# Optimization experiments

Measured on AMD Instinct MI355X. Metric: run time of the kernel, lower is better.

Reference implementation:

```python
import jax, jax.numpy as jnp
import numpy as np

D_MODEL = 768
N_CH = 2
D_STATE = 16
RANK = 8
LORA_SCALE = 2.0  # alpha/rank = (rank*2.0)/rank
N_LOOPS = 4       # MAX_INFER_LOOPS
BATCH = 1
SEQ = 1024
EPS = 1e-6        # RMSNorm eps


def setup_inputs() -> dict:
    key = jax.random.key(0)
    ks = jax.random.split(key, 12)
    f32 = jnp.float32
    n = lambda k, shp, s: jax.random.normal(k, shp, dtype=f32) * s
    return {
        "x": jax.random.normal(ks[0], (BATCH, SEQ, D_MODEL), dtype=f32),
        "in_proj_base": n(ks[1], (N_CH * D_MODEL, D_MODEL), 0.02),
        "lora_A": n(ks[2], (RANK, D_MODEL), 0.05),
        "lora_B": n(ks[3], (N_CH * D_MODEL, RANK), 0.05),
        "A_theta": n(ks[4], (N_CH, D_MODEL, D_STATE), 0.1),
        "B_real": n(ks[5], (N_CH, D_MODEL, D_STATE), 0.1),
        "B_imag": n(ks[6], (N_CH, D_MODEL, D_STATE), 0.1),
        "C_real": n(ks[7], (N_CH, D_MODEL, D_STATE), 0.1),
        "C_imag": n(ks[8], (N_CH, D_MODEL, D_STATE), 0.1),
        "out_proj_w": n(ks[9], (D_MODEL, N_CH * D_MODEL), 0.02),
        "mixer_norm_w": jnp.ones((D_MODEL,), f32),
        "loop_norm_w": jnp.ones((D_MODEL,), f32),
        "step_emb": n(ks[10], (N_LOOPS, D_MODEL), 0.02),
    }


def _rmsnorm(v, w):
    return v * jax.lax.rsqrt(jnp.mean(v * v, axis=-1, keepdims=True) + EPS) * w


def reference(x, in_proj_base, lora_A, lora_B, A_theta, B_real, B_imag,
              C_real, C_imag, out_proj_w, mixer_norm_w, loop_norm_w, step_emb):
    Bsz, Lsz, d = x.shape
    # LoRA-merged in_proj weight: base + scale * (B @ A)  [loop-invariant]
    W_in = in_proj_base + LORA_SCALE * (lora_B @ lora_A)  # [2d, d]
    cos_t = jnp.cos(A_theta)[None, None]  # [1,1,ch,d,s]
    sin_t = jnp.sin(A_theta)[None, None]
    Br = B_real[None, None]; Bi = B_imag[None, None]
    Cr = C_real[None, None]; Ci = C_imag[None, None]
    real = jnp.zeros((Bsz, Lsz, N_CH, d, D_STATE), x.dtype)
    imag = jnp.zeros_like(real)
    for i in range(N_LOOPS):  # fixed outer reasoning loop
        h = x + step_emb[i]
        # Mamba3ReasoningBlock: in_proj -> complex rotation state update -> sum over d_state
        x_in = (h @ W_in.T).reshape(Bsz, Lsz, N_CH, d)[..., None]  # [B,L,ch,d,1]
        new_real = cos_t * real - sin_t * imag + Br * x_in
        new_imag = sin_t * real + cos_t * imag + Bi * x_in
        y = (Cr * new_real - Ci * new_imag).sum(-1).reshape(Bsz, Lsz, N_CH * d)
        out = _rmsnorm(y @ out_proj_w.T, mixer_norm_w)
        x = _rmsnorm(h + out, loop_norm_w)  # residual + loop_norm
        real, imag = new_real, new_imag
    return x
```

## Files before the change

kernel.cpp:

```cpp
#include <hip/hip_runtime.h>

#define D_MODEL   768
#define TWO_D     1536
#define SEQ       1024
#define N_LOOPS   4
#define RANK      8
#define D_STATE   16
#define EPS       1e-6f

typedef unsigned short u16;
typedef short s16x8 __attribute__((ext_vector_type(8)));
typedef unsigned short u16x4 __attribute__((ext_vector_type(4)));
typedef float f32x4 __attribute__((ext_vector_type(4)));

__device__ inline u16 f2bf(float f) {
    union { float f; unsigned u; } v; v.f = f;
    unsigned r = v.u + 0x7fffu + ((v.u >> 16) & 1u);
    return (u16)(r >> 16);
}
__device__ inline float bf2f(u16 b) {
    union { unsigned u; float f; } v; v.u = ((unsigned)b) << 16;
    return v.f;
}

__global__ __launch_bounds__(256) void prep_win(
    const float* __restrict__ base, const float* __restrict__ lA,
    const float* __restrict__ lB, u16* __restrict__ W)
{
    int idx = blockIdx.x * 256 + threadIdx.x;
    int r = idx / D_MODEL;
    int c = idx - r * D_MODEL;
    float acc = base[idx];
#pragma unroll
    for (int k = 0; k < RANK; ++k)
        acc += 2.0f * lB[r * RANK + k] * lA[k * D_MODEL + c];
    W[idx] = f2bf(acc);
}

__global__ __launch_bounds__(256) void prep_wout(
    const float* __restrict__ src, u16* __restrict__ dst)
{
    int i4 = blockIdx.x * 256 + threadIdx.x;
    const float4 v = *reinterpret_cast<const float4*>(src + (size_t)i4 * 4);
    u16x4 o; o.x = f2bf(v.x); o.y = f2bf(v.y); o.z = f2bf(v.z); o.w = f2bf(v.w);
    *reinterpret_cast<u16x4*>(dst + (size_t)i4 * 4) = o;
}

__global__ __launch_bounds__(256) void prep_g(
    const float* __restrict__ th, const float* __restrict__ Br,
    const float* __restrict__ Bi, const float* __restrict__ Cr,
    const float* __restrict__ Ci, float* __restrict__ G)
{
    int cd = blockIdx.x * 256 + threadIdx.x;
    if (cd >= TWO_D) return;
    float g0 = 0.f, g1 = 0.f, g2 = 0.f, g3 = 0.f;
    for (int s = 0; s < D_STATE; ++s) {
        int idx = cd * D_STATE + s;
        float t  = th[idx];
        float br = Br[idx], bi = Bi[idx];
        float cr = Cr[idx], ci = Ci[idx];
#pragma unroll
        for (int k = 0; k < 4; ++k) {
            float ck = cosf(k * t), sk = sinf(k * t);
            float er = ck * br - sk * bi;
            float ei = sk * br + ck * bi;
            float g  = cr * er - ci * ei;
            if (k == 0) g0 += g; else if (k == 1) g1 += g;
            else if (k == 2) g2 += g; else g3 += g;
        }
    }
    G[0 * TWO_D + cd] = g0;
    G[1 * TWO_D + cd] = g1;
    G[2 * TWO_D + cd] = g2;
    G[3 * TWO_D + cd] = g3;
}

__global__ __launch_bounds__(256) void init_h(
    const float* __restrict__ x, const float* __restrict__ emb,
    float* __restrict__ hf, u16* __restrict__ hb)
{
    int i4 = blockIdx.x * 256 + threadIdx.x;
    int base = i4 * 4;
    int d = base % D_MODEL;
    const float4 v = *reinterpret_cast<const float4*>(x + base);
    const float4 e = *reinterpret_cast<const float4*>(emb + d);
    float4 h = make_float4(v.x + e.x, v.y + e.y, v.z + e.z, v.w + e.w);
    *reinterpret_cast<float4*>(hf + base) = h;
    u16x4 o; o.x = f2bf(h.x); o.y = f2bf(h.y); o.z = f2bf(h.z); o.w = f2bf(h.w);
    *reinterpret_cast<u16x4*>(hb + base) = o;
}

template<int K, bool OUT_BF16>
__global__ __launch_bounds__(256) void gemm_nt(
    const u16* __restrict__ A, const u16* __restrict__ B,
    void* __restrict__ Cv, const int N)
{
    __shared__ u16 Al[64][72];
    __shared__ u16 Bl[64][72];
    const int t  = threadIdx.x;
    const int bm = blockIdx.y, bn = blockIdx.x;
    const int lane = t & 63, w = t >> 6;
    const int wr = w >> 1, wc = w & 1;
    const int lr = lane & 15, kg = lane >> 4;

    const int r0 = t >> 3;
    const int q0 = t & 7;
    const u16* Ag0 = A + (size_t)(bm * 64 + r0)      * K + q0 * 8;
    const u16* Ag1 = A + (size_t)(bm * 64 + r0 + 32) * K + q0 * 8;
    const u16* Bg0 = B + (size_t)(bn * 64 + r0)      * K + q0 * 8;
    const u16* Bg1 = B + (size_t)(bn * 64 + r0 + 32) * K + q0 * 8;

    uint4 ra0 = *reinterpret_cast<const uint4*>(Ag0);
    uint4 ra1 = *reinterpret_cast<const uint4*>(Ag1);
    uint4 rb0 = *reinterpret_cast<const uint4*>(Bg0);
    uint4 rb1 = *reinterpret_cast<const uint4*>(Bg1);

    f32x4 acc[2][2] = {};
    const int NKT = K / 64;
    for (int kt = 0; kt < NKT; ++kt) {
        *reinterpret_cast<uint4*>(&Al[r0][q0 * 8])      = ra0;
        *reinterpret_cast<uint4*>(&Al[r0 + 32][q0 * 8]) = ra1;
        *reinterpret_cast<uint4*>(&Bl[r0][q0 * 8])      = rb0;
        *reinterpret_cast<uint4*>(&Bl[r0 + 32][q0 * 8]) = rb1;
        __syncthreads();
        if (kt + 1 < NKT) {
            const int ko = (kt + 1) * 64;
            ra0 = *reinterpret_cast<const uint4*>(Ag0 + ko);
            ra1 = *reinterpret_cast<const uint4*>(Ag1 + ko);
            rb0 = *reinterpret_cast<const uint4*>(Bg0 + ko);
            rb1 = *reinterpret_cast<const uint4*>(Bg1 + ko);
        }
#pragma unroll
        for (int ks = 0; ks < 2; ++ks) {
            const int ko = ks * 32 + kg * 8;
            s16x8 a0 = *reinterpret_cast<const s16x8*>(&Al[wr * 32 + lr][ko]);
            s16x8 a1 = *reinterpret_cast<const s16x8*>(&Al[wr * 32 + 16 + lr][ko]);
            s16x8 b0 = *reinterpret_cast<const s16x8*>(&Bl[wc * 32 + lr][ko]);
            s16x8 b1 = *reinterpret_cast<const s16x8*>(&Bl[wc * 32 + 16 + lr][ko]);
            acc[0][0] = __builtin_amdgcn_mfma_f32_16x16x32_bf16(a0, b0, acc[0][0], 0, 0, 0);
            acc[0][1] = __builtin_amdgcn_mfma_f32_16x16x32_bf16(a0, b1, acc[0][1], 0, 0, 0);
            acc[1][0] = __builtin_amdgcn_mfma_f32_16x16x32_bf16(a1, b0, acc[1][0], 0, 0, 0);
            acc[1][1] = __builtin_amdgcn_mfma_f32_16x16x32_bf16(a1, b1, acc[1][1], 0, 0, 0);
        }
        __syncthreads();
    }
    const int crow0 = bm * 64 + wr * 32 + kg * 4;
    const int ccol0 = bn * 64 + wc * 32 + lr;
#pragma unroll
    for (int m = 0; m < 2; ++m)
#pragma unroll
        for (int n = 0; n < 2; ++n)
#pragma unroll
            for (int r = 0; r < 4; ++r) {
                const int row = crow0 + m * 16 + r;
                const int col = ccol0 + n * 16;
                const float v = acc[m][n][r];
                if (OUT_BF16) ((u16*)Cv)[(size_t)row * N + col] = f2bf(v);
                else          ((float*)Cv)[(size_t)row * N + col] = v;
            }
}

__global__ __launch_bounds__(256) void y_kernel(
    const u16* __restrict__ xin,
    const float* __restrict__ G,
    const int nacc, u16* __restrict__ y)
{
    int i4 = blockIdx.x * 256 + threadIdx.x;
    int base = i4 * 4;
    int cd = base % TWO_D;
    float s0 = 0.f, s1 = 0.f, s2 = 0.f, s3 = 0.f;
    for (int j = 0; j < nacc; ++j) {
        u16x4 v = *reinterpret_cast<const u16x4*>(&xin[(size_t)j * SEQ * TWO_D + base]);
        const float4 g = *reinterpret_cast<const float4*>(&G[(size_t)(nacc - 1 - j) * TWO_D + cd]);
        s0 += bf2f(v.x) * g.x; s1 += bf2f(v.y) * g.y;
        s2 += bf2f(v.z) * g.z; s3 += bf2f(v.w) * g.w;
    }
    u16x4 o; o.x = f2bf(s0); o.y = f2bf(s1); o.z = f2bf(s2); o.w = f2bf(s3);
    *reinterpret_cast<u16x4*>(&y[base]) = o;
}

__device__ inline float block_sum256(float v) {
    __shared__ float sm[4];
#pragma unroll
    for (int off = 32; off > 0; off >>= 1) v += __shfl_down(v, off, 64);
    __syncthreads();
    if ((threadIdx.x & 63) == 0) sm[threadIdx.x >> 6] = v;
    __syncthreads();
    return sm[0] + sm[1] + sm[2] + sm[3];
}

__global__ __launch_bounds__(256) void norm_kernel(
    const float* __restrict__ outpre,
    const float* __restrict__ hprev,
    const float* __restrict__ mw,
    const float* __restrict__ lw,
    const float* __restrict__ embn,
    float* __restrict__ dstf,
    u16* __restrict__ dstb)
{
    const int r = blockIdx.x;
    const int t = threadIdx.x;
    const size_t ro = (size_t)r * D_MODEL;
    float op[3], h[3];
    float ss = 0.f;
#pragma unroll
    for (int j = 0; j < 3; ++j) {
        int d = t + j * 256;
        op[j] = outpre[ro + d];
        h[j]  = hprev[ro + d];
        ss += op[j] * op[j];
    }
    ss = block_sum256(ss);
    const float rs1 = rsqrtf(ss * (1.0f / D_MODEL) + EPS);
    float tt[3];
    float ss2 = 0.f;
#pragma unroll
    for (int j = 0; j < 3; ++j) {
        int d = t + j * 256;
        tt[j] = h[j] + op[j] * rs1 * mw[d];
        ss2 += tt[j] * tt[j];
    }
    ss2 = block_sum256(ss2);
    const float rs2 = rsqrtf(ss2 * (1.0f / D_MODEL) + EPS);
#pragma unroll
    for (int j = 0; j < 3; ++j) {
        int d = t + j * 256;
        float xo = tt[j] * rs2 * lw[d];
        if (embn != nullptr) {
            float hn = xo + embn[d];
            dstf[ro + d] = hn;
            dstb[ro + d] = f2bf(hn);
        } else {
            dstf[ro + d] = xo;
        }
    }
}

extern "C" void kernel_launch(void* const* d_in, const int* in_sizes, int n_in,
                              void* d_out, int out_size, void* d_ws, size_t ws_size,
                              hipStream_t stream) {
    const float* x            = (const float*)d_in[0];
    const float* in_proj_base = (const float*)d_in[1];
    const float* lora_A       = (const float*)d_in[2];
    const float* lora_B       = (const float*)d_in[3];
    const float* A_theta      = (const float*)d_in[4];
    const float* B_real       = (const float*)d_in[5];
    const float* B_imag       = (const float*)d_in[6];
    const float* C_real       = (const float*)d_in[7];
    const float* C_imag       = (const float*)d_in[8];
    const float* out_proj_w   = (const float*)d_in[9];
    const float* mixer_w      = (const float*)d_in[10];
    const float* loop_w       = (const float*)d_in[11];
    const float* step_emb     = (const float*)d_in[12];
    float* out = (float*)d_out;

    char* p = (char*)d_ws;
    u16*   Wbf    = (u16*)p;                       p += (size_t)TWO_D * D_MODEL * 2;
    u16*   Woutbf = (u16*)p;                       p += (size_t)D_MODEL * TWO_D * 2;
    float* G      = (float*)p;                     p += (size_t)4 * TWO_D * 4;
    u16*   xin    = (u16*)p;                       p += (size_t)N_LOOPS * SEQ * TWO_D * 2;
    u16*   ybf    = (u16*)p;                       p += (size_t)SEQ * TWO_D * 2;
    float* hAf    = (float*)p;                     p += (size_t)SEQ * D_MODEL * 4;
    float* hBf    = (float*)p;                     p += (size_t)SEQ * D_MODEL * 4;
    u16*   hbf    = (u16*)p;                       p += (size_t)SEQ * D_MODEL * 2;
    float* outpre = (float*)p;                     p += (size_t)SEQ * D_MODEL * 4;

    prep_win<<<(TWO_D * D_MODEL) / 256, 256, 0, stream>>>(in_proj_base, lora_A, lora_B, Wbf);
    prep_wout<<<(D_MODEL * TWO_D / 4) / 256, 256, 0, stream>>>(out_proj_w, Woutbf);
    prep_g<<<(TWO_D + 255) / 256, 256, 0, stream>>>(A_theta, B_real, B_imag, C_real, C_imag, G);
    init_h<<<(SEQ * D_MODEL / 4) / 256, 256, 0, stream>>>(x, step_emb, hAf, hbf);

    float* hcur = hAf;
    float* hnxt = hBf;
    for (int i = 0; i < N_LOOPS; ++i) {
        const bool last = (i == N_LOOPS - 1);
        gemm_nt<D_MODEL, true><<<dim3(TWO_D / 64, SEQ / 64), 256, 0, stream>>>(
            hbf, Wbf, (void*)(xin + (size_t)i * SEQ * TWO_D), TWO_D);
        y_kernel<<<(SEQ * TWO_D / 4) / 256, 256, 0, stream>>>(xin, G, i + 1, ybf);
        gemm_nt<TWO_D, false><<<dim3(D_MODEL / 64, SEQ / 64), 256, 0, stream>>>(
            ybf, Woutbf, (void*)outpre, D_MODEL);
        norm_kernel<<<SEQ, 256, 0, stream>>>(
            outpre, hcur, mixer_w, loop_w,
            last ? nullptr : (step_emb + (size_t)(i + 1) * D_MODEL),
            last ? out : hnxt,
            last ? nullptr : hbf);
        float* tmp = hcur; hcur = hnxt; hnxt = tmp;
    }
}
```

Baseline: 244.5 us.

## Fuse prep kernels, fold y accumulation into GEMM1 epilogue, split-K GEMM2

Merges the four setup kernels into one launch, and folds the y recurrence into the epilogue of the in_proj GEMM so the separate y kernel disappears. Both GEMMs now use a 128-wide K tile with padded shared memory. The out_proj GEMM is split along K into two partial outputs that the norm kernel adds together, doubling its grid from 192 blocks to fill more CUs. In exchange there is an extra fp32 partial buffer, and the new epilogue does scalar strided reads of older xin slots and of G.

```diff
diff --git a/kernel.cpp b/kernel.cpp
--- a/kernel.cpp
+++ b/kernel.cpp
@@ -7,6 +7,8 @@
 #define RANK      8
 #define D_STATE   16
 #define EPS       1e-6f
+#define BK        128
+#define LDA       136
 
 typedef unsigned short u16;
 typedef short s16x8 __attribute__((ext_vector_type(8)));
@@ -23,120 +25,118 @@
     return v.f;
 }
 
-__global__ __launch_bounds__(256) void prep_win(
+__global__ __launch_bounds__(256) void prep_all(
     const float* __restrict__ base, const float* __restrict__ lA,
-    const float* __restrict__ lB, u16* __restrict__ W)
-{
-    int idx = blockIdx.x * 256 + threadIdx.x;
-    int r = idx / D_MODEL;
-    int c = idx - r * D_MODEL;
-    float acc = base[idx];
-#pragma unroll
-    for (int k = 0; k < RANK; ++k)
-        acc += 2.0f * lB[r * RANK + k] * lA[k * D_MODEL + c];
-    W[idx] = f2bf(acc);
-}
-
-__global__ __launch_bounds__(256) void prep_wout(
-    const float* __restrict__ src, u16* __restrict__ dst)
-{
-    int i4 = blockIdx.x * 256 + threadIdx.x;
-    const float4 v = *reinterpret_cast<const float4*>(src + (size_t)i4 * 4);
-    u16x4 o; o.x = f2bf(v.x); o.y = f2bf(v.y); o.z = f2bf(v.z); o.w = f2bf(v.w);
-    *reinterpret_cast<u16x4*>(dst + (size_t)i4 * 4) = o;
-}
-
-__global__ __launch_bounds__(256) void prep_g(
-    const float* __restrict__ th, const float* __restrict__ Br,
-    const float* __restrict__ Bi, const float* __restrict__ Cr,
-    const float* __restrict__ Ci, float* __restrict__ G)
-{
-    int cd = blockIdx.x * 256 + threadIdx.x;
-    if (cd >= TWO_D) return;
-    float g0 = 0.f, g1 = 0.f, g2 = 0.f, g3 = 0.f;
-    for (int s = 0; s < D_STATE; ++s) {
-        int idx = cd * D_STATE + s;
-        float t  = th[idx];
-        float br = Br[idx], bi = Bi[idx];
-        float cr = Cr[idx], ci = Ci[idx];
-#pragma unroll
-        for (int k = 0; k < 4; ++k) {
-            float ck = cosf(k * t), sk = sinf(k * t);
-            float er = ck * br - sk * bi;
-            float ei = sk * br + ck * bi;
-            float g  = cr * er - ci * ei;
-            if (k == 0) g0 += g; else if (k == 1) g1 += g;
-            else if (k == 2) g2 += g; else g3 += g;
-        }
-    }
-    G[0 * TWO_D + cd] = g0;
-    G[1 * TWO_D + cd] = g1;
-    G[2 * TWO_D + cd] = g2;
-    G[3 * TWO_D + cd] = g3;
-}
-
-__global__ __launch_bounds__(256) void init_h(
-    const float* __restrict__ x, const float* __restrict__ emb,
+    const float* __restrict__ lB,   const float* __restrict__ wout,
+    const float* __restrict__ x,    const float* __restrict__ emb0,
+    const float* __restrict__ th,   const float* __restrict__ Br,
+    const float* __restrict__ Bi,   const float* __restrict__ Cr,
+    const float* __restrict__ Ci,
+    u16* __restrict__ Wbf, u16* __restrict__ Woutbf, float* __restrict__ G,
     float* __restrict__ hf, u16* __restrict__ hb)
 {
-    int i4 = blockIdx.x * 256 + threadIdx.x;
-    int base = i4 * 4;
-    int d = base % D_MODEL;
-    const float4 v = *reinterpret_cast<const float4*>(x + base);
-    const float4 e = *reinterpret_cast<const float4*>(emb + d);
-    float4 h = make_float4(v.x + e.x, v.y + e.y, v.z + e.z, v.w + e.w);
-    *reinterpret_cast<float4*>(hf + base) = h;
-    u16x4 o; o.x = f2bf(h.x); o.y = f2bf(h.y); o.z = f2bf(h.z); o.w = f2bf(h.w);
-    *reinterpret_cast<u16x4*>(hb + base) = o;
-}
-
-template<int K, bool OUT_BF16>
-__global__ __launch_bounds__(256) void gemm_nt(
-    const u16* __restrict__ A, const u16* __restrict__ B,
-    void* __restrict__ Cv, const int N)
+    const int b = blockIdx.x, t = threadIdx.x;
+    if (b < 1152) {
+        int i0 = (b * 256 + t) * 4;
+        int r = i0 / D_MODEL, c = i0 % D_MODEL;
+        float4 a = *reinterpret_cast<const float4*>(&base[i0]);
+#pragma unroll
+        for (int k = 0; k < RANK; ++k) {
+            float bk = 2.0f * lB[r * RANK + k];
+            const float4 av = *reinterpret_cast<const float4*>(&lA[k * D_MODEL + c]);
+            a.x += bk * av.x; a.y += bk * av.y; a.z += bk * av.z; a.w += bk * av.w;
+        }
+        u16x4 o; o.x = f2bf(a.x); o.y = f2bf(a.y); o.z = f2bf(a.z); o.w = f2bf(a.w);
+        *reinterpret_cast<u16x4*>(&Wbf[i0]) = o;
+    } else if (b < 2304) {
+        int i0 = ((b - 1152) * 256 + t) * 4;
+        const float4 v = *reinterpret_cast<const float4*>(&wout[i0]);
+        u16x4 o; o.x = f2bf(v.x); o.y = f2bf(v.y); o.z = f2bf(v.z); o.w = f2bf(v.w);
+        *reinterpret_cast<u16x4*>(&Woutbf[i0]) = o;
+    } else if (b < 3072) {
+        int i0 = ((b - 2304) * 256 + t) * 4;
+        int d = i0 % D_MODEL;
+        const float4 v = *reinterpret_cast<const float4*>(&x[i0]);
+        const float4 e = *reinterpret_cast<const float4*>(&emb0[d]);
+        float4 h = make_float4(v.x + e.x, v.y + e.y, v.z + e.z, v.w + e.w);
+        *reinterpret_cast<float4*>(&hf[i0]) = h;
+        u16x4 o; o.x = f2bf(h.x); o.y = f2bf(h.y); o.z = f2bf(h.z); o.w = f2bf(h.w);
+        *reinterpret_cast<u16x4*>(&hb[i0]) = o;
+    } else {
+        int cd = (b - 3072) * 256 + t;
+        if (cd >= TWO_D) return;
+        float g0 = 0.f, g1 = 0.f, g2 = 0.f, g3 = 0.f;
+        for (int s = 0; s < D_STATE; ++s) {
+            int idx = cd * D_STATE + s;
+            float tt = th[idx];
+            float br = Br[idx], bi = Bi[idx];
+            float cr = Cr[idx], ci = Ci[idx];
+#pragma unroll
+            for (int k = 0; k < 4; ++k) {
+                float ck = cosf(k * tt), sk = sinf(k * tt);
+                float er = ck * br - sk * bi;
+                float ei = sk * br + ck * bi;
+                float g  = cr * er - ci * ei;
+                if (k == 0) g0 += g; else if (k == 1) g1 += g;
+                else if (k == 2) g2 += g; else g3 += g;
+            }
+        }
+        G[0 * TWO_D + cd] = g0; G[1 * TWO_D + cd] = g1;
+        G[2 * TWO_D + cd] = g2; G[3 * TWO_D + cd] = g3;
+    }
+}
+
+__global__ __launch_bounds__(256) void gemm1y_kernel(
+    const u16* __restrict__ A,
+    const u16* __restrict__ B,
+    u16* __restrict__ xin,
+    u16* __restrict__ ybf,
+    const float* __restrict__ G,
+    const int li)
 {
-    __shared__ u16 Al[64][72];
-    __shared__ u16 Bl[64][72];
-    const int t  = threadIdx.x;
-    const int bm = blockIdx.y, bn = blockIdx.x;
+    __shared__ __align__(16) u16 Al[64 * LDA];
+    __shared__ __align__(16) u16 Bl[64 * LDA];
+    const int K = D_MODEL;
+    const int t = threadIdx.x, bm = blockIdx.y, bn = blockIdx.x;
     const int lane = t & 63, w = t >> 6;
     const int wr = w >> 1, wc = w & 1;
     const int lr = lane & 15, kg = lane >> 4;
 
-    const int r0 = t >> 3;
-    const int q0 = t & 7;
-    const u16* Ag0 = A + (size_t)(bm * 64 + r0)      * K + q0 * 8;
-    const u16* Ag1 = A + (size_t)(bm * 64 + r0 + 32) * K + q0 * 8;
-    const u16* Bg0 = B + (size_t)(bn * 64 + r0)      * K + q0 * 8;
-    const u16* Bg1 = B + (size_t)(bn * 64 + r0 + 32) * K + q0 * 8;
-
-    uint4 ra0 = *reinterpret_cast<const uint4*>(Ag0);
-    uint4 ra1 = *reinterpret_cast<const uint4*>(Ag1);
-    uint4 rb0 = *reinterpret_cast<const uint4*>(Bg0);
-    uint4 rb1 = *reinterpret_cast<const uint4*>(Bg1);
-
+    const u16* Ab = A + (size_t)bm * 64 * K;
+    const u16* Bb = B + (size_t)bn * 64 * K;
+    uint4 pa[4], pb[4];
+#pragma unroll
+    for (int q = 0; q < 4; ++q) {
+        int gid = q * 256 + t, row = gid >> 4, g = gid & 15;
+        pa[q] = *reinterpret_cast<const uint4*>(Ab + (size_t)row * K + g * 8);
+        pb[q] = *reinterpret_cast<const uint4*>(Bb + (size_t)row * K + g * 8);
+    }
     f32x4 acc[2][2] = {};
-    const int NKT = K / 64;
+    const int NKT = K / BK;
     for (int kt = 0; kt < NKT; ++kt) {
-        *reinterpret_cast<uint4*>(&Al[r0][q0 * 8])      = ra0;
-        *reinterpret_cast<uint4*>(&Al[r0 + 32][q0 * 8]) = ra1;
-        *reinterpret_cast<uint4*>(&Bl[r0][q0 * 8])      = rb0;
-        *reinterpret_cast<uint4*>(&Bl[r0 + 32][q0 * 8]) = rb1;
+#pragma unroll
+        for (int q = 0; q < 4; ++q) {
+            int gid = q * 256 + t, row = gid >> 4, g = gid & 15;
+            *reinterpret_cast<uint4*>(&Al[row * LDA + g * 8]) = pa[q];
+            *reinterpret_cast<uint4*>(&Bl[row * LDA + g * 8]) = pb[q];
+        }
         __syncthreads();
         if (kt + 1 < NKT) {
-            const int ko = (kt + 1) * 64;
-            ra0 = *reinterpret_cast<const uint4*>(Ag0 + ko);
-            ra1 = *reinterpret_cast<const uint4*>(Ag1 + ko);
-            rb0 = *reinterpret_cast<const uint4*>(Bg0 + ko);
-            rb1 = *reinterpret_cast<const uint4*>(Bg1 + ko);
-        }
-#pragma unroll
-        for (int ks = 0; ks < 2; ++ks) {
-            const int ko = ks * 32 + kg * 8;
-            s16x8 a0 = *reinterpret_cast<const s16x8*>(&Al[wr * 32 + lr][ko]);
-            s16x8 a1 = *reinterpret_cast<const s16x8*>(&Al[wr * 32 + 16 + lr][ko]);
-            s16x8 b0 = *reinterpret_cast<const s16x8*>(&Bl[wc * 32 + lr][ko]);
-            s16x8 b1 = *reinterpret_cast<const s16x8*>(&Bl[wc * 32 + 16 + lr][ko]);
+            const int ko = (kt + 1) * BK;
+#pragma unroll
+            for (int q = 0; q < 4; ++q) {
+                int gid = q * 256 + t, row = gid >> 4, g = gid & 15;
+                pa[q] = *reinterpret_cast<const uint4*>(Ab + (size_t)row * K + ko + g * 8);
+                pb[q] = *reinterpret_cast<const uint4*>(Bb + (size_t)row * K + ko + g * 8);
+            }
+        }
+#pragma unroll
+        for (int ks = 0; ks < BK / 32; ++ks) {
+            const int co = ks * 32 + kg * 8;
+            s16x8 a0 = *reinterpret_cast<const s16x8*>(&Al[(wr * 32 +      lr) * LDA + co]);
+            s16x8 a1 = *reinterpret_cast<const s16x8*>(&Al[(wr * 32 + 16 + lr) * LDA + co]);
+            s16x8 b0 = *reinterpret_cast<const s16x8*>(&Bl[(wc * 32 +      lr) * LDA + co]);
+            s16x8 b1 = *reinterpret_cast<const s16x8*>(&Bl[(wc * 32 + 16 + lr) * LDA + co]);
             acc[0][0] = __builtin_amdgcn_mfma_f32_16x16x32_bf16(a0, b0, acc[0][0], 0, 0, 0);
             acc[0][1] = __builtin_amdgcn_mfma_f32_16x16x32_bf16(a0, b1, acc[0][1], 0, 0, 0);
             acc[1][0] = __builtin_amdgcn_mfma_f32_16x16x32_bf16(a1, b0, acc[1][0], 0, 0, 0);
@@ -146,37 +146,93 @@
     }
     const int crow0 = bm * 64 + wr * 32 + kg * 4;
     const int ccol0 = bn * 64 + wc * 32 + lr;
-#pragma unroll
-    for (int m = 0; m < 2; ++m)
-#pragma unroll
-        for (int n = 0; n < 2; ++n)
+    u16* xslot = xin + (size_t)li * SEQ * TWO_D;
+#pragma unroll
+    for (int n = 0; n < 2; ++n) {
+        const int col = ccol0 + n * 16;
+        const float g0 = G[col];
+#pragma unroll
+        for (int m = 0; m < 2; ++m)
 #pragma unroll
             for (int r = 0; r < 4; ++r) {
                 const int row = crow0 + m * 16 + r;
-                const int col = ccol0 + n * 16;
+                const size_t off = (size_t)row * TWO_D + col;
                 const float v = acc[m][n][r];
-                if (OUT_BF16) ((u16*)Cv)[(size_t)row * N + col] = f2bf(v);
-                else          ((float*)Cv)[(size_t)row * N + col] = v;
+                xslot[off] = f2bf(v);
+                float y = g0 * v;
+                for (int j = 0; j < li; ++j)
+                    y += G[(size_t)(li - j) * TWO_D + col] *
+                         bf2f(xin[(size_t)j * SEQ * TWO_D + off]);
+                ybf[off] = f2bf(y);
             }
-}
-
-__global__ __launch_bounds__(256) void y_kernel(
-    const u16* __restrict__ xin,
-    const float* __restrict__ G,
-    const int nacc, u16* __restrict__ y)
+    }
+}
+
+__global__ __launch_bounds__(256) void gemm2_kernel(
+    const u16* __restrict__ A,
+    const u16* __restrict__ B,
+    float* __restrict__ Cp)
 {
-    int i4 = blockIdx.x * 256 + threadIdx.x;
-    int base = i4 * 4;
-    int cd = base % TWO_D;
-    float s0 = 0.f, s1 = 0.f, s2 = 0.f, s3 = 0.f;
-    for (int j = 0; j < nacc; ++j) {
-        u16x4 v = *reinterpret_cast<const u16x4*>(&xin[(size_t)j * SEQ * TWO_D + base]);
-        const float4 g = *reinterpret_cast<const float4*>(&G[(size_t)(nacc - 1 - j) * TWO_D + cd]);
-        s0 += bf2f(v.x) * g.x; s1 += bf2f(v.y) * g.y;
-        s2 += bf2f(v.z) * g.z; s3 += bf2f(v.w) * g.w;
-    }
-    u16x4 o; o.x = f2bf(s0); o.y = f2bf(s1); o.z = f2bf(s2); o.w = f2bf(s3);
-    *reinterpret_cast<u16x4*>(&y[base]) = o;
+    __shared__ __align__(16) u16 Al[64 * LDA];
+    __shared__ __align__(16) u16 Bl[64 * LDA];
+    const int K = TWO_D;
+    const int t = threadIdx.x, bm = blockIdx.y, bn = blockIdx.x, kz = blockIdx.z;
+    const int lane = t & 63, w = t >> 6;
+    const int wr = w >> 1, wc = w & 1;
+    const int lr = lane & 15, kg = lane >> 4;
+
+    const u16* Ab = A + (size_t)bm * 64 * K + kz * (K / 2);
+    const u16* Bb = B + (size_t)bn * 64 * K + kz * (K / 2);
+    uint4 pa[4], pb[4];
+#pragma unroll
+    for (int q = 0; q < 4; ++q) {
+        int gid = q * 256 + t, row = gid >> 4, g = gid & 15;
+        pa[q] = *reinterpret_cast<const uint4*>(Ab + (size_t)row * K + g * 8);
+        pb[q] = *reinterpret_cast<const uint4*>(Bb + (size_t)row * K + g * 8);
+    }
+    f32x4 acc[2][2] = {};
+    const int NKT = (K / 2) / BK;
+    for (int kt = 0; kt < NKT; ++kt) {
+#pragma unroll
+        for (int q = 0; q < 4; ++q) {
+            int gid = q * 256 + t, row = gid >> 4, g = gid & 15;
+            *reinterpret_cast<uint4*>(&Al[row * LDA + g * 8]) = pa[q];
+            *reinterpret_cast<uint4*>(&Bl[row * LDA + g * 8]) = pb[q];
+        }
+        __syncthreads();
+        if (kt + 1 < NKT) {
+            const int ko = (kt + 1) * BK;
+#pragma unroll
+            for (int q = 0; q < 4; ++q) {
+                int gid = q * 256 + t, row = gid >> 4, g = gid & 15;
+                pa[q] = *reinterpret_cast<const uint4*>(Ab + (size_t)row * K + ko + g * 8);
+                pb[q] = *reinterpret_cast<const uint4*>(Bb + (size_t)row * K + ko + g * 8);
+            }
+        }
+#pragma unroll
+        for (int ks = 0; ks < BK / 32; ++ks) {
+            const int co = ks * 32 + kg * 8;
+            s16x8 a0 = *reinterpret_cast<const s16x8*>(&Al[(wr * 32 +      lr) * LDA + co]);
+            s16x8 a1 = *reinterpret_cast<const s16x8*>(&Al[(wr * 32 + 16 + lr) * LDA + co]);
+            s16x8 b0 = *reinterpret_cast<const s16x8*>(&Bl[(wc * 32 +      lr) * LDA + co]);
+            s16x8 b1 = *reinterpret_cast<const s16x8*>(&Bl[(wc * 32 + 16 + lr) * LDA + co]);
+            acc[0][0] = __builtin_amdgcn_mfma_f32_16x16x32_bf16(a0, b0, acc[0][0], 0, 0, 0);
+            acc[0][1] = __builtin_amdgcn_mfma_f32_16x16x32_bf16(a0, b1, acc[0][1], 0, 0, 0);
+            acc[1][0] = __builtin_amdgcn_mfma_f32_16x16x32_bf16(a1, b0, acc[1][0], 0, 0, 0);
+            acc[1][1] = __builtin_amdgcn_mfma_f32_16x16x32_bf16(a1, b1, acc[1][1], 0, 0, 0);
+        }
+        __syncthreads();
+    }
+    const int crow0 = bm * 64 + wr * 32 + kg * 4;
+    const int ccol0 = bn * 64 + wc * 32 + lr;
+    float* Cz = Cp + (size_t)kz * SEQ * D_MODEL;
+#pragma unroll
+    for (int m = 0; m < 2; ++m)
+#pragma unroll
+        for (int n = 0; n < 2; ++n)
+#pragma unroll
+            for (int r = 0; r < 4; ++r)
+                Cz[(size_t)(crow0 + m * 16 + r) * D_MODEL + ccol0 + n * 16] = acc[m][n][r];
 }
 
 __device__ inline float block_sum256(float v) {
@@ -190,13 +246,11 @@
 }
 
 __global__ __launch_bounds__(256) void norm_kernel(
-    const float* __restrict__ outpre,
+    const float* __restrict__ op0, const float* __restrict__ op1,
     const float* __restrict__ hprev,
-    const float* __restrict__ mw,
-    const float* __restrict__ lw,
+    const float* __restrict__ mw,  const float* __restrict__ lw,
     const float* __restrict__ embn,
-    float* __restrict__ dstf,
-    u16* __restrict__ dstb)
+    float* __restrict__ dstf, u16* __restrict__ dstb)
 {
     const int r = blockIdx.x;
     const int t = threadIdx.x;
@@ -206,7 +260,7 @@
 #pragma unroll
     for (int j = 0; j < 3; ++j) {
         int d = t + j * 256;
-        op[j] = outpre[ro + d];
+        op[j] = op0[ro + d] + op1[ro + d];
         h[j]  = hprev[ro + d];
         ss += op[j] * op[j];
     }
@@ -255,32 +309,31 @@
     float* out = (float*)d_out;
 
     char* p = (char*)d_ws;
-    u16*   Wbf    = (u16*)p;                       p += (size_t)TWO_D * D_MODEL * 2;
-    u16*   Woutbf = (u16*)p;                       p += (size_t)D_MODEL * TWO_D * 2;
-    float* G      = (float*)p;                     p += (size_t)4 * TWO_D * 4;
-    u16*   xin    = (u16*)p;                       p += (size_t)N_LOOPS * SEQ * TWO_D * 2;
-    u16*   ybf    = (u16*)p;                       p += (size_t)SEQ * TWO_D * 2;
-    float* hAf    = (float*)p;                     p += (size_t)SEQ * D_MODEL * 4;
-    float* hBf    = (float*)p;                     p += (size_t)SEQ * D_MODEL * 4;
-    u16*   hbf    = (u16*)p;                       p += (size_t)SEQ * D_MODEL * 2;
-    float* outpre = (float*)p;                     p += (size_t)SEQ * D_MODEL * 4;
-
-    prep_win<<<(TWO_D * D_MODEL) / 256, 256, 0, stream>>>(in_proj_base, lora_A, lora_B, Wbf);
-    prep_wout<<<(D_MODEL * TWO_D / 4) / 256, 256, 0, stream>>>(out_proj_w, Woutbf);
-    prep_g<<<(TWO_D + 255) / 256, 256, 0, stream>>>(A_theta, B_real, B_imag, C_real, C_imag, G);
-    init_h<<<(SEQ * D_MODEL / 4) / 256, 256, 0, stream>>>(x, step_emb, hAf, hbf);
+    u16*   Wbf    = (u16*)p;   p += (size_t)TWO_D * D_MODEL * 2;
+    u16*   Woutbf = (u16*)p;   p += (size_t)D_MODEL * TWO_D * 2;
+    float* G      = (float*)p; p += (size_t)4 * TWO_D * 4;
+    u16*   xin    = (u16*)p;   p += (size_t)N_LOOPS * SEQ * TWO_D * 2;
+    u16*   ybf    = (u16*)p;   p += (size_t)SEQ * TWO_D * 2;
+    float* hAf    = (float*)p; p += (size_t)SEQ * D_MODEL * 4;
+    float* hBf    = (float*)p; p += (size_t)SEQ * D_MODEL * 4;
+    u16*   hbf    = (u16*)p;   p += (size_t)SEQ * D_MODEL * 2;
+    float* outpre = (float*)p; p += (size_t)2 * SEQ * D_MODEL * 4;
+
+    prep_all<<<3078, 256, 0, stream>>>(
+        in_proj_base, lora_A, lora_B, out_proj_w, x, step_emb,
+        A_theta, B_real, B_imag, C_real, C_imag,
+        Wbf, Woutbf, G, hAf, hbf);
 
     float* hcur = hAf;
     float* hnxt = hBf;
     for (int i = 0; i < N_LOOPS; ++i) {
         const bool last = (i == N_LOOPS - 1);
-        gemm_nt<D_MODEL, true><<<dim3(TWO_D / 64, SEQ / 64), 256, 0, stream>>>(
-            hbf, Wbf, (void*)(xin + (size_t)i * SEQ * TWO_D), TWO_D);
-        y_kernel<<<(SEQ * TWO_D / 4) / 256, 256, 0, stream>>>(xin, G, i + 1, ybf);
-        gemm_nt<TWO_D, false><<<dim3(D_MODEL / 64, SEQ / 64), 256, 0, stream>>>(
-            ybf, Woutbf, (void*)outpre, D_MODEL);
+        gemm1y_kernel<<<dim3(TWO_D / 64, SEQ / 64), 256, 0, stream>>>(
+            hbf, Wbf, xin, ybf, G, i);
+        gemm2_kernel<<<dim3(D_MODEL / 64, SEQ / 64, 2), 256, 0, stream>>>(
+            ybf, Woutbf, outpre);
         norm_kernel<<<SEQ, 256, 0, stream>>>(
-            outpre, hcur, mixer_w, loop_w,
+            outpre, outpre + (size_t)SEQ * D_MODEL, hcur, mixer_w, loop_w,
             last ? nullptr : (step_emb + (size_t)(i + 1) * D_MODEL),
             last ? out : hnxt,
             last ? nullptr : hbf);
```

Result: slower. 369.8 us (+51.2%).

## Fuse prep kernels, split-K out_proj GEMM, wave-per-row norm

Applied to the files above, without the earlier changes.

Merges the four one-time preparation kernels into a single launch that dispatches on block index, and vectorizes the LoRA merge with float4 loads. The out_proj GEMM now splits K in two across blockIdx.z, doubling the grid from 192 to 384 blocks so more CUs are busy, and writes two partial fp32 outputs. The norm kernel sums the two partials and gives each row to one wavefront, using shuffle reductions in place of shared-memory block reductions. The split-K adds an extra fp32 buffer to write and read back, plus the summation work in the norm.

```diff
diff --git a/kernel.cpp b/kernel.cpp
--- a/kernel.cpp
+++ b/kernel.cpp
@@ -23,74 +23,68 @@
     return v.f;
 }
 
-__global__ __launch_bounds__(256) void prep_win(
+__global__ __launch_bounds__(256) void prep_all(
     const float* __restrict__ base, const float* __restrict__ lA,
-    const float* __restrict__ lB, u16* __restrict__ W)
-{
-    int idx = blockIdx.x * 256 + threadIdx.x;
-    int r = idx / D_MODEL;
-    int c = idx - r * D_MODEL;
-    float acc = base[idx];
-#pragma unroll
-    for (int k = 0; k < RANK; ++k)
-        acc += 2.0f * lB[r * RANK + k] * lA[k * D_MODEL + c];
-    W[idx] = f2bf(acc);
-}
-
-__global__ __launch_bounds__(256) void prep_wout(
-    const float* __restrict__ src, u16* __restrict__ dst)
-{
-    int i4 = blockIdx.x * 256 + threadIdx.x;
-    const float4 v = *reinterpret_cast<const float4*>(src + (size_t)i4 * 4);
-    u16x4 o; o.x = f2bf(v.x); o.y = f2bf(v.y); o.z = f2bf(v.z); o.w = f2bf(v.w);
-    *reinterpret_cast<u16x4*>(dst + (size_t)i4 * 4) = o;
-}
-
-__global__ __launch_bounds__(256) void prep_g(
-    const float* __restrict__ th, const float* __restrict__ Br,
-    const float* __restrict__ Bi, const float* __restrict__ Cr,
-    const float* __restrict__ Ci, float* __restrict__ G)
-{
-    int cd = blockIdx.x * 256 + threadIdx.x;
-    if (cd >= TWO_D) return;
-    float g0 = 0.f, g1 = 0.f, g2 = 0.f, g3 = 0.f;
-    for (int s = 0; s < D_STATE; ++s) {
-        int idx = cd * D_STATE + s;
-        float t  = th[idx];
-        float br = Br[idx], bi = Bi[idx];
-        float cr = Cr[idx], ci = Ci[idx];
-#pragma unroll
-        for (int k = 0; k < 4; ++k) {
-            float ck = cosf(k * t), sk = sinf(k * t);
-            float er = ck * br - sk * bi;
-            float ei = sk * br + ck * bi;
-            float g  = cr * er - ci * ei;
-            if (k == 0) g0 += g; else if (k == 1) g1 += g;
-            else if (k == 2) g2 += g; else g3 += g;
-        }
-    }
-    G[0 * TWO_D + cd] = g0;
-    G[1 * TWO_D + cd] = g1;
-    G[2 * TWO_D + cd] = g2;
-    G[3 * TWO_D + cd] = g3;
-}
-
-__global__ __launch_bounds__(256) void init_h(
-    const float* __restrict__ x, const float* __restrict__ emb,
+    const float* __restrict__ lB,   const float* __restrict__ wout,
+    const float* __restrict__ x,    const float* __restrict__ emb0,
+    const float* __restrict__ th,   const float* __restrict__ Br,
+    const float* __restrict__ Bi,   const float* __restrict__ Cr,
+    const float* __restrict__ Ci,
+    u16* __restrict__ Wbf, u16* __restrict__ Woutbf, float* __restrict__ G,
     float* __restrict__ hf, u16* __restrict__ hb)
 {
-    int i4 = blockIdx.x * 256 + threadIdx.x;
-    int base = i4 * 4;
-    int d = base % D_MODEL;
-    const float4 v = *reinterpret_cast<const float4*>(x + base);
-    const float4 e = *reinterpret_cast<const float4*>(emb + d);
-    float4 h = make_float4(v.x + e.x, v.y + e.y, v.z + e.z, v.w + e.w);
-    *reinterpret_cast<float4*>(hf + base) = h;
-    u16x4 o; o.x = f2bf(h.x); o.y = f2bf(h.y); o.z = f2bf(h.z); o.w = f2bf(h.w);
-    *reinterpret_cast<u16x4*>(hb + base) = o;
-}
-
-template<int K, bool OUT_BF16>
+    const int b = blockIdx.x, t = threadIdx.x;
+    if (b < 1152) {
+        int i0 = (b * 256 + t) * 4;
+        int r = i0 / D_MODEL, c = i0 % D_MODEL;
+        float4 a = *reinterpret_cast<const float4*>(&base[i0]);
+#pragma unroll
+        for (int k = 0; k < RANK; ++k) {
+            float bk = 2.0f * lB[r * RANK + k];
+            const float4 av = *reinterpret_cast<const float4*>(&lA[k * D_MODEL + c]);
+            a.x += bk * av.x; a.y += bk * av.y; a.z += bk * av.z; a.w += bk * av.w;
+        }
+        u16x4 o; o.x = f2bf(a.x); o.y = f2bf(a.y); o.z = f2bf(a.z); o.w = f2bf(a.w);
+        *reinterpret_cast<u16x4*>(&Wbf[i0]) = o;
+    } else if (b < 2304) {
+        int i0 = ((b - 1152) * 256 + t) * 4;
+        const float4 v = *reinterpret_cast<const float4*>(&wout[i0]);
+        u16x4 o; o.x = f2bf(v.x); o.y = f2bf(v.y); o.z = f2bf(v.z); o.w = f2bf(v.w);
+        *reinterpret_cast<u16x4*>(&Woutbf[i0]) = o;
+    } else if (b < 3072) {
+        int i0 = ((b - 2304) * 256 + t) * 4;
+        int d = i0 % D_MODEL;
+        const float4 v = *reinterpret_cast<const float4*>(&x[i0]);
+        const float4 e = *reinterpret_cast<const float4*>(&emb0[d]);
+        float4 h = make_float4(v.x + e.x, v.y + e.y, v.z + e.z, v.w + e.w);
+        *reinterpret_cast<float4*>(&hf[i0]) = h;
+        u16x4 o; o.x = f2bf(h.x); o.y = f2bf(h.y); o.z = f2bf(h.z); o.w = f2bf(h.w);
+        *reinterpret_cast<u16x4*>(&hb[i0]) = o;
+    } else {
+        int cd = (b - 3072) * 256 + t;
+        if (cd >= TWO_D) return;
+        float g0 = 0.f, g1 = 0.f, g2 = 0.f, g3 = 0.f;
+        for (int s = 0; s < D_STATE; ++s) {
+            int idx = cd * D_STATE + s;
+            float tt = th[idx];
+            float br = Br[idx], bi = Bi[idx];
+            float cr = Cr[idx], ci = Ci[idx];
+#pragma unroll
+            for (int k = 0; k < 4; ++k) {
+                float ck = cosf(k * tt), sk = sinf(k * tt);
+                float er = ck * br - sk * bi;
+                float ei = sk * br + ck * bi;
+                float g  = cr * er - ci * ei;
+                if (k == 0) g0 += g; else if (k == 1) g1 += g;
+                else if (k == 2) g2 += g; else g3 += g;
+            }
+        }
+        G[0 * TWO_D + cd] = g0; G[1 * TWO_D + cd] = g1;
+        G[2 * TWO_D + cd] = g2; G[3 * TWO_D + cd] = g3;
+    }
+}
+
+template<int K, int SPLITK, bool OUT_BF16>
 __global__ __launch_bounds__(256) void gemm_nt(
     const u16* __restrict__ A, const u16* __restrict__ B,
     void* __restrict__ Cv, const int N)
@@ -98,17 +92,20 @@
     __shared__ u16 Al[64][72];
     __shared__ u16 Bl[64][72];
     const int t  = threadIdx.x;
-    const int bm = blockIdx.y, bn = blockIdx.x;
+    const int bm = blockIdx.y, bn = blockIdx.x, kz = blockIdx.z;
     const int lane = t & 63, w = t >> 6;
     const int wr = w >> 1, wc = w & 1;
     const int lr = lane & 15, kg = lane >> 4;
 
+    const int KS = K / SPLITK;
+    const int kbase = kz * KS;
+
     const int r0 = t >> 3;
     const int q0 = t & 7;
-    const u16* Ag0 = A + (size_t)(bm * 64 + r0)      * K + q0 * 8;
-    const u16* Ag1 = A + (size_t)(bm * 64 + r0 + 32) * K + q0 * 8;
-    const u16* Bg0 = B + (size_t)(bn * 64 + r0)      * K + q0 * 8;
-    const u16* Bg1 = B + (size_t)(bn * 64 + r0 + 32) * K + q0 * 8;
+    const u16* Ag0 = A + (size_t)(bm * 64 + r0)      * K + kbase + q0 * 8;
+    const u16* Ag1 = A + (size_t)(bm * 64 + r0 + 32) * K + kbase + q0 * 8;
+    const u16* Bg0 = B + (size_t)(bn * 64 + r0)      * K + kbase + q0 * 8;
+    const u16* Bg1 = B + (size_t)(bn * 64 + r0 + 32) * K + kbase + q0 * 8;
 
     uint4 ra0 = *reinterpret_cast<const uint4*>(Ag0);
     uint4 ra1 = *reinterpret_cast<const uint4*>(Ag1);
@@ -116,7 +113,7 @@
     uint4 rb1 = *reinterpret_cast<const uint4*>(Bg1);
 
     f32x4 acc[2][2] = {};
-    const int NKT = K / 64;
+    const int NKT = KS / 64;
     for (int kt = 0; kt < NKT; ++kt) {
         *reinterpret_cast<uint4*>(&Al[r0][q0 * 8])      = ra0;
         *reinterpret_cast<uint4*>(&Al[r0 + 32][q0 * 8]) = ra1;
@@ -156,7 +153,7 @@
                 const int col = ccol0 + n * 16;
                 const float v = acc[m][n][r];
                 if (OUT_BF16) ((u16*)Cv)[(size_t)row * N + col] = f2bf(v);
-                else          ((float*)Cv)[(size_t)row * N + col] = v;
+                else ((float*)Cv)[(size_t)kz * SEQ * N + (size_t)row * N + col] = v;
             }
 }
 
@@ -179,53 +176,43 @@
     *reinterpret_cast<u16x4*>(&y[base]) = o;
 }
 
-__device__ inline float block_sum256(float v) {
-    __shared__ float sm[4];
-#pragma unroll
-    for (int off = 32; off > 0; off >>= 1) v += __shfl_down(v, off, 64);
-    __syncthreads();
-    if ((threadIdx.x & 63) == 0) sm[threadIdx.x >> 6] = v;
-    __syncthreads();
-    return sm[0] + sm[1] + sm[2] + sm[3];
-}
-
 __global__ __launch_bounds__(256) void norm_kernel(
-    const float* __restrict__ outpre,
+    const float* __restrict__ op0, const float* __restrict__ op1,
     const float* __restrict__ hprev,
-    const float* __restrict__ mw,
-    const float* __restrict__ lw,
+    const float* __restrict__ mw,  const float* __restrict__ lw,
     const float* __restrict__ embn,
-    float* __restrict__ dstf,
-    u16* __restrict__ dstb)
-{
-    const int r = blockIdx.x;
-    const int t = threadIdx.x;
+    float* __restrict__ dstf, u16* __restrict__ dstb)
+{
+    const int r = blockIdx.x * 4 + (threadIdx.x >> 6);
+    const int lane = threadIdx.x & 63;
     const size_t ro = (size_t)r * D_MODEL;
-    float op[3], h[3];
+    float op[12], h[12];
     float ss = 0.f;
 #pragma unroll
-    for (int j = 0; j < 3; ++j) {
-        int d = t + j * 256;
-        op[j] = outpre[ro + d];
-        h[j]  = hprev[ro + d];
-        ss += op[j] * op[j];
-    }
-    ss = block_sum256(ss);
+    for (int e = 0; e < 12; ++e) {
+        int d = lane + e * 64;
+        op[e] = op0[ro + d] + op1[ro + d];
+        h[e]  = hprev[ro + d];
+        ss += op[e] * op[e];
+    }
+#pragma unroll
+    for (int off = 32; off > 0; off >>= 1) ss += __shfl_xor(ss, off, 64);
     const float rs1 = rsqrtf(ss * (1.0f / D_MODEL) + EPS);
-    float tt[3];
+    float tt[12];
     float ss2 = 0.f;
 #pragma unroll
-    for (int j = 0; j < 3; ++j) {
-        int d = t + j * 256;
-        tt[j] = h[j] + op[j] * rs1 * mw[d];
-        ss2 += tt[j] * tt[j];
-    }
-    ss2 = block_sum256(ss2);
+    for (int e = 0; e < 12; ++e) {
+        int d = lane + e * 64;
+        tt[e] = h[e] + op[e] * rs1 * mw[d];
+        ss2 += tt[e] * tt[e];
+    }
+#pragma unroll
+    for (int off = 32; off > 0; off >>= 1) ss2 += __shfl_xor(ss2, off, 64);
     const float rs2 = rsqrtf(ss2 * (1.0f / D_MODEL) + EPS);
 #pragma unroll
-    for (int j = 0; j < 3; ++j) {
-        int d = t + j * 256;
-        float xo = tt[j] * rs2 * lw[d];
+    for (int e = 0; e < 12; ++e) {
+        int d = lane + e * 64;
+        float xo = tt[e] * rs2 * lw[d];
         if (embn != nullptr) {
             float hn = xo + embn[d];
             dstf[ro + d] = hn;
@@ -255,32 +242,32 @@
     float* out = (float*)d_out;
 
     char* p = (char*)d_ws;
-    u16*   Wbf    = (u16*)p;                       p += (size_t)TWO_D * D_MODEL * 2;
-    u16*   Woutbf = (u16*)p;                       p += (size_t)D_MODEL * TWO_D * 2;
-    float* G      = (float*)p;                     p += (size_t)4 * TWO_D * 4;
-    u16*   xin    = (u16*)p;                       p += (size_t)N_LOOPS * SEQ * TWO_D * 2;
-    u16*   ybf    = (u16*)p;                       p += (size_t)SEQ * TWO_D * 2;
-    float* hAf    = (float*)p;                     p += (size_t)SEQ * D_MODEL * 4;
-    float* hBf    = (float*)p;                     p += (size_t)SEQ * D_MODEL * 4;
-    u16*   hbf    = (u16*)p;                       p += (size_t)SEQ * D_MODEL * 2;
-    float* outpre = (float*)p;                     p += (size_t)SEQ * D_MODEL * 4;
-
-    prep_win<<<(TWO_D * D_MODEL) / 256, 256, 0, stream>>>(in_proj_base, lora_A, lora_B, Wbf);
-    prep_wout<<<(D_MODEL * TWO_D / 4) / 256, 256, 0, stream>>>(out_proj_w, Woutbf);
-    prep_g<<<(TWO_D + 255) / 256, 256, 0, stream>>>(A_theta, B_real, B_imag, C_real, C_imag, G);
-    init_h<<<(SEQ * D_MODEL / 4) / 256, 256, 0, stream>>>(x, step_emb, hAf, hbf);
+    u16*   Wbf    = (u16*)p;   p += (size_t)TWO_D * D_MODEL * 2;
+    u16*   Woutbf = (u16*)p;   p += (size_t)D_MODEL * TWO_D * 2;
+    float* G      = (float*)p; p += (size_t)4 * TWO_D * 4;
+    u16*   xin    = (u16*)p;   p += (size_t)N_LOOPS * SEQ * TWO_D * 2;
+    u16*   ybf    = (u16*)p;   p += (size_t)SEQ * TWO_D * 2;
+    float* hAf    = (float*)p; p += (size_t)SEQ * D_MODEL * 4;
+    float* hBf    = (float*)p; p += (size_t)SEQ * D_MODEL * 4;
+    u16*   hbf    = (u16*)p;   p += (size_t)SEQ * D_MODEL * 2;
+    float* outpre = (float*)p; p += (size_t)2 * SEQ * D_MODEL * 4;
+
+    prep_all<<<3078, 256, 0, stream>>>(
+        in_proj_base, lora_A, lora_B, out_proj_w, x, step_emb,
+        A_theta, B_real, B_imag, C_real, C_imag,
+        Wbf, Woutbf, G, hAf, hbf);
 
     float* hcur = hAf;
     float* hnxt = hBf;
     for (int i = 0; i < N_LOOPS; ++i) {
         const bool last = (i == N_LOOPS - 1);
-        gemm_nt<D_MODEL, true><<<dim3(TWO_D / 64, SEQ / 64), 256, 0, stream>>>(
+        gemm_nt<D_MODEL, 1, true><<<dim3(TWO_D / 64, SEQ / 64), 256, 0, stream>>>(
             hbf, Wbf, (void*)(xin + (size_t)i * SEQ * TWO_D), TWO_D);
         y_kernel<<<(SEQ * TWO_D / 4) / 256, 256, 0, stream>>>(xin, G, i + 1, ybf);
-        gemm_nt<TWO_D, false><<<dim3(D_MODEL / 64, SEQ / 64), 256, 0, stream>>>(
+        gemm_nt<TWO_D, 2, false><<<dim3(D_MODEL / 64, SEQ / 64, 2), 256, 0, stream>>>(
             ybf, Woutbf, (void*)outpre, D_MODEL);
-        norm_kernel<<<SEQ, 256, 0, stream>>>(
-            outpre, hcur, mixer_w, loop_w,
+        norm_kernel<<<SEQ / 4, 256, 0, stream>>>(
+            outpre, outpre + (size_t)SEQ * D_MODEL, hcur, mixer_w, loop_w,
             last ? nullptr : (step_emb + (size_t)(i + 1) * D_MODEL),
             last ? out : hnxt,
             last ? nullptr : hbf);
```

New measurement: 228.7 us. 1.07x faster.
